# Kernel tuning notes

Measured on AMD Instinct MI355X. Metric: run time of the kernel, lower is better.

## Reference

```python
import jax, jax.numpy as jnp
import numpy as np

N_VERT = 20000


def _gather_pad(feat, adj):
    # feat: [B, N, C]; adj: [B, N, K] with 1-based indices, 0 = padding (-> zeros)
    B, N, C = feat.shape
    padded = jnp.concatenate([jnp.zeros((B, 1, C), feat.dtype), feat], axis=1)  # [B, N+1, C]
    return jax.vmap(lambda p, a: p[a])(padded, adj)  # [B, N, K, C]


def setup_inputs() -> dict:
    key = jax.random.key(0)
    ks = jax.random.split(key, 7)
    B, N, K, M, C, O = 4, N_VERT, 16, 9, 64, 64
    x = jax.random.normal(ks[0], (B, N, C), jnp.float32)
    adj = jax.random.randint(ks[1], (B, N, K), 0, N + 1, jnp.int32)  # 0 == no neighbor
    W = jax.random.normal(ks[2], (M, O, C), jnp.float32) * 0.1
    b = jax.random.normal(ks[3], (O,), jnp.float32) * 0.1
    u = jax.random.normal(ks[4], (M, C), jnp.float32) * 0.1
    v = jax.random.normal(ks[5], (M, C), jnp.float32) * 0.1
    c = jax.random.normal(ks[6], (M,), jnp.float32) * 0.1
    return {"x": x, "adj": adj, "W": W, "b": b, "u": u, "v": v, "c": c}


def reference(x, adj, W, b, u, v, c):
    # FEAST graph conv, non-invariant path.
    mask = adj != 0  # [B, N, K]
    # attention logits: u.x_i + v.x_j + c, masked (padding) neighbors -> 0 + c
    ux = jnp.einsum('bnc,mc->bnm', x, u)          # [B, N, M]
    vx = jnp.einsum('bnc,mc->bnm', x, v)          # [B, N, M]
    vxn = _gather_pad(vx, adj)                    # [B, N, K, M]
    logits = jnp.where(mask[..., None], ux[:, :, None, :] + vxn, 0.0) + c
    q = jax.nn.softmax(logits, axis=-1)           # softmax over M kernels
    # gather raw neighbor features (zero for padding), contract q over K first,
    # then apply per-kernel W (linear, so order is equivalent to original wx-gather)
    xn = _gather_pad(x, adj)                      # [B, N, K, C]
    s = jnp.einsum('bnkm,bnkc->bnmc', q, xn)      # [B, N, M, C]
    out = jnp.einsum('bnmc,moc->bno', s, W)       # [B, N, O]
    deg = jnp.sum(mask, axis=-1).astype(x.dtype)  # [B, N]
    inv_deg = jnp.where(deg > 0, 1.0 / jnp.maximum(deg, 1.0), 0.0)
    return out * inv_deg[..., None] + b
```

## Files before the change

### kernel.cpp

```cpp
#include <hip/hip_runtime.h>
#include <cstdint>
#include <cstddef>

#define BB 4
#define NN 20000
#define KK 16
#define MM 9
#define CC 64
#define OO 64
#define BN (BB*NN)
#define MC (MM*CC)
#define UVP 12
#define NKS (MC/32)
#define NCH 625

typedef _Float16 f16x8 __attribute__((ext_vector_type(8)));
typedef _Float16 f16x4 __attribute__((ext_vector_type(4)));
typedef __fp16   fp16v2 __attribute__((ext_vector_type(2)));
typedef float    f32x4 __attribute__((ext_vector_type(4)));
typedef unsigned short u16;
typedef unsigned int   u32;

union Hcv { _Float16 h; u16 u; };
__device__ __forceinline__ u16 f2h(float f) { Hcv t; t.h = (_Float16)f; return t.u; }
__device__ __forceinline__ float h2f(u16 h) { Hcv t; t.u = h; return (float)t.h; }

__device__ __forceinline__ f16x4 tr_read(u32 addr) {
    f16x4 r;
    asm volatile("ds_read_b64_tr_b16 %0, %1 offset:0" : "=v"(r) : "v"(addr) : "memory");
    return r;
}

__global__ __launch_bounds__(256) void pre_kernel(
    const float* __restrict__ x, const float* __restrict__ W,
    const float* __restrict__ u, const float* __restrict__ v,
    const float* __restrict__ c,
    float* __restrict__ uxcv, u16* __restrict__ xh,
    u16* __restrict__ wfb2, u16* __restrict__ vfa)
{
    const int bid = blockIdx.x;
    if (bid == 1286) {
        int i0 = threadIdx.x * 4;
        if (i0 < 1024) {
            u16 w4[4];
            #pragma unroll
            for (int tt = 0; tt < 4; ++tt) {
                int i = i0 + tt;
                int l = i >> 4, s = (i >> 3) & 1, j = i & 7;
                int m = l & 15, hh = l >> 4;
                float val = (m < 9) ? v[m * 64 + s * 32 + hh * 8 + j] : 0.f;
                w4[tt] = f2h(val);
            }
            *(ushort4*)(vfa + i0) = *(ushort4*)(w4);
        }
        return;
    }
    if (bid >= 1250) {
        int base = (bid - 1250) * 1024 + threadIdx.x * 4;
        ushort4 wv;
        u16* wp = (u16*)&wv;
        #pragma unroll
        for (int t = 0; t < 4; ++t) {
            int i = base + t;
            int j = i & 7, o = (i >> 3) & 63, l2 = (i >> 9) & 3, ks = i >> 11;
            int kf = ks * 32 + l2 * 8 + j;
            int m = kf >> 6, cc2 = kf & 63;
            wp[t] = f2h(W[m * 4096 + o * 64 + cc2]);
        }
        *(ushort4*)(wfb2 + base) = wv;
        return;
    }
    const int wave = threadIdx.x >> 6, lane = threadIdx.x & 63;
    const int lr = lane & 15, lhi = lane >> 4;
    const int t0n = bid * 64 + wave * 16;
    const float* xr = x + (size_t)(t0n + lr) * 64 + lhi * 8;
    float xf[16];
    *(float4*)(xf + 0)  = *(const float4*)(xr + 0);
    *(float4*)(xf + 4)  = *(const float4*)(xr + 4);
    *(float4*)(xf + 8)  = *(const float4*)(xr + 32);
    *(float4*)(xf + 12) = *(const float4*)(xr + 36);
    union { u16 us[8]; f16x8 v; ushort4 s4[2]; } H0, L0, H1, L1;
    #pragma unroll
    for (int i = 0; i < 8; ++i) {
        u16 h = f2h(xf[i]);      H0.us[i] = h;  L0.us[i] = f2h(xf[i] - h2f(h));
        u16 h2 = f2h(xf[8 + i]); H1.us[i] = h2; L1.us[i] = f2h(xf[8 + i] - h2f(h2));
    }
    u16* xw = xh + (size_t)(t0n + lr) * 64 + lhi * 8;
    *(ushort4*)(xw)          = H0.s4[0];
    *(ushort4*)(xw + 4)      = H0.s4[1];
    *(ushort4*)(xw + 32)     = H1.s4[0];
    *(ushort4*)(xw + 32 + 4) = H1.s4[1];

    f32x4 acc = {0.f,0.f,0.f,0.f};
    const float* gp = u + lr * 64;
    bool nz = lr < 9;
    #pragma unroll
    for (int s = 0; s < 2; ++s) {
        float gf[8];
        *(float4*)(gf + 0) = nz ? *(const float4*)(gp + s * 32 + lhi * 8)
                                : make_float4(0.f,0.f,0.f,0.f);
        *(float4*)(gf + 4) = nz ? *(const float4*)(gp + s * 32 + lhi * 8 + 4)
                                : make_float4(0.f,0.f,0.f,0.f);
        union { u16 us[8]; f16x8 v; } GH, GL;
        #pragma unroll
        for (int i = 0; i < 8; ++i) {
            u16 h = f2h(gf[i]); GH.us[i] = h; GL.us[i] = f2h(gf[i] - h2f(h));
        }
        f16x8 as  = s ? H1.v : H0.v;
        f16x8 asl = s ? L1.v : L0.v;
        acc = __builtin_amdgcn_mfma_f32_16x16x32_f16(as,  GH.v, acc, 0, 0, 0);
        acc = __builtin_amdgcn_mfma_f32_16x16x32_f16(as,  GL.v, acc, 0, 0, 0);
        acc = __builtin_amdgcn_mfma_f32_16x16x32_f16(asl, GH.v, acc, 0, 0, 0);
    }
    float cv = (lr < 9) ? c[lr] : 0.f;
    #pragma unroll
    for (int reg = 0; reg < 4; ++reg) {
        int node = t0n + lhi * 4 + reg;
        if (lr < 9) uxcv[(size_t)node * UVP + lr] = acc[reg] + cv;
    }
}

__global__ __launch_bounds__(256, 2) void fused_kernel(
    const u16* __restrict__ xh, const int* __restrict__ adj,
    const float* __restrict__ uxcv, const u16* __restrict__ wfb2,
    const u16* __restrict__ vfa, const float* __restrict__ bias,
    float* __restrict__ out)
{
    __shared__ __align__(16) u16 qlds[4 * 4 * 256];
    __shared__ __align__(16) u16 xnlds[4 * 4 * 1024];
    __shared__ __align__(16) u16 slds[72 * 32 * 8];
    const int bid = blockIdx.x;
    const int grp = bid & 7;
    const int b = grp >> 1;
    const int chunk = (bid >> 3) * 2 + (grp & 1);
    if (chunk >= NCH) return;
    const int tid = threadIdx.x, wave = tid >> 6, lane = tid & 63;
    const int lr = lane & 15, lhi = lane >> 4;
    const int node0 = b * NN + chunk * 32;
    const u16* xhb = xh + ((size_t)(b * NN) << 6);

    int jjA[2];
    jjA[0] = adj[(size_t)node0 * KK + tid];
    jjA[1] = adj[(size_t)node0 * KK + 256 + tid];

    f16x8 gLo[2][4], gHi[2][4];
    #pragma unroll
    for (int t = 0; t < 2; ++t)
        #pragma unroll
        for (int g2 = 0; g2 < 4; ++g2) {
            int e = __builtin_amdgcn_ds_bpermute((g2 * 16 + lr) * 4, jjA[t]);
            int erow = ((e > 0) ? e : 1) - 1;
            const u16* rp = xhb + ((size_t)erow << 6) + lhi * 8;
            gLo[t][g2] = *(const f16x8*)(rp);
            gHi[t][g2] = *(const f16x8*)(rp + 32);
        }

    float4 uc[2][4];
    #pragma unroll
    for (int t = 0; t < 2; ++t)
        #pragma unroll
        for (int g2 = 0; g2 < 4; ++g2)
            uc[t][g2] = *(const float4*)(uxcv +
                          (size_t)(node0 + t * 16 + wave * 4 + g2) * UVP + lhi * 4);

    const u16* vp = vfa + lane * 16;
    const f16x8 vAlo = *(const f16x8*)(vp);
    const f16x8 vAhi = *(const f16x8*)(vp + 8);

    const int o0 = wave * 16;
    const float bv = bias[o0 + lr];
    const u32 qbase  = (u32)(size_t)qlds  + wave * 2048 + lane * 8;
    const u32 xnbase = (u32)(size_t)xnlds + wave * 8192 + lane * 8;
    u16* xnw = xnlds + wave * 4096 + (lhi >> 1) * 256 + lr * 16 + (lhi & 1) * 8;
    u16* qwp = qlds + wave * 1024 + lhi * 4 + (lr & 3) * 16 + (lr >> 2) * 64;

    #pragma unroll
    for (int t = 0; t < 2; ++t) {
        unsigned long long bal = __ballot(jjA[t] != 0);
        #pragma unroll
        for (int g2 = 0; g2 < 4; ++g2) {
            *(f16x8*)(xnw + g2 * 1024)       = gLo[t][g2];
            *(f16x8*)(xnw + g2 * 1024 + 512) = gHi[t][g2];
        }
        #pragma unroll
        for (int g2 = 0; g2 < 4; ++g2) {
            f32x4 acc = {0.f, 0.f, 0.f, 0.f};
            acc = __builtin_amdgcn_mfma_f32_16x16x32_f16(vAlo, gLo[t][g2], acc, 0, 0, 0);
            acc = __builtin_amdgcn_mfma_f32_16x16x32_f16(vAhi, gHi[t][g2], acc, 0, 0, 0);
            u32 field = (u32)(bal >> (g2 * 16)) & 0xffffu;
            int  deg  = __popc(field);
            float inv = (deg > 0) ? __fdividef(1.0f, (float)deg) : 0.0f;
            int kbit = (field >> lr) & 1;
            float lm[4];
            #pragma unroll
            for (int r = 0; r < 4; ++r)
                lm[r] = (lhi * 4 + r < 9) ? (acc[r] + ((const float*)&uc[t][g2])[r])
                                          : -1e30f;
            float mx = fmaxf(fmaxf(lm[0], lm[1]), fmaxf(lm[2], lm[3]));
            mx = fmaxf(mx, __shfl_xor(mx, 16));
            mx = fmaxf(mx, __shfl_xor(mx, 32));
            float p0 = __expf(lm[0] - mx), p1 = __expf(lm[1] - mx);
            float p2 = __expf(lm[2] - mx), p3 = __expf(lm[3] - mx);
            float S = p0 + p1 + p2 + p3;
            S += __shfl_xor(S, 16);
            S += __shfl_xor(S, 32);
            float qsc = kbit ? __fdividef(inv, S) : 0.0f;
            union { fp16v2 h2[2]; uint2 u2; } qp;
            qp.h2[0] = __builtin_amdgcn_cvt_pkrtz(p0 * qsc, p1 * qsc);
            qp.h2[1] = __builtin_amdgcn_cvt_pkrtz(p2 * qsc, p3 * qsc);
            *(uint2*)(qwp + g2 * 256) = qp.u2;
        }
        asm volatile("s_waitcnt lgkmcnt(0)" ::: "memory");
        __builtin_amdgcn_sched_barrier(0);
        f16x4 qf[4], xnf[4][4];
        #pragma unroll
        for (int g2 = 0; g2 < 4; ++g2) {
            qf[g2] = tr_read(qbase + g2 * 512);
            #pragma unroll
            for (int cc = 0; cc < 4; ++cc)
                xnf[g2][cc] = tr_read(xnbase + g2 * 2048 + cc * 512);
        }
        asm volatile("s_waitcnt lgkmcnt(0)" ::: "memory");
        __builtin_amdgcn_sched_barrier(0);
        #pragma unroll
        for (int g2 = 0; g2 < 4; ++g2) {
            const int rnode = t * 16 + wave * 4 + g2;
            #pragma unroll
            for (int cc = 0; cc < 4; ++cc) {
                f32x4 d2 = {0.f, 0.f, 0.f, 0.f};
                d2 = __builtin_amdgcn_mfma_f32_16x16x16f16(xnf[g2][cc], qf[g2], d2, 0, 0, 0);
                if (lr < 9) {
                    u32 lo = __builtin_amdgcn_perm((u32)f2h(d2[1]), (u32)f2h(d2[0]), 0x05040100u);
                    u32 hi = __builtin_amdgcn_perm((u32)f2h(d2[3]), (u32)f2h(d2[2]), 0x05040100u);
                    int q_ = lr * 8 + cc * 2 + (lhi >> 1);
                    int idx = (((q_ * 32 + rnode) << 3) ^ ((lr & 7) << 3)) + (lhi & 1) * 4;
                    *(uint2*)(slds + idx) = make_uint2(lo, hi);
                }
            }
        }
    }
    __syncthreads();

    f32x4 a0 = {0.f, 0.f, 0.f, 0.f}, a1 = {0.f, 0.f, 0.f, 0.f};
    #pragma unroll
    for (int ks = 0; ks < NKS; ++ks) {
        int q_ = ks * 4 + lhi;
        int sw = ((q_ >> 3) & 7) << 3;
        f16x8 af0 = *(const f16x8*)(slds + ((((q_ * 32) + lr) << 3) ^ sw));
        f16x8 af1 = *(const f16x8*)(slds + ((((q_ * 32) + 16 + lr) << 3) ^ sw));
        f16x8 bf  = *(const f16x8*)(wfb2 + (size_t)(q_ * 64 + o0 + lr) * 8);
        a0 = __builtin_amdgcn_mfma_f32_16x16x32_f16(af0, bf, a0, 0, 0, 0);
        a1 = __builtin_amdgcn_mfma_f32_16x16x32_f16(af1, bf, a1, 0, 0, 0);
    }
    #pragma unroll
    for (int r = 0; r < 4; ++r) {
        out[(size_t)(node0 + lhi * 4 + r) * OO + o0 + lr]      = a0[r] + bv;
        out[(size_t)(node0 + 16 + lhi * 4 + r) * OO + o0 + lr] = a1[r] + bv;
    }
}

extern "C" void kernel_launch(void* const* d_in, const int* in_sizes, int n_in,
                              void* d_out, int out_size, void* d_ws, size_t ws_size,
                              hipStream_t stream)
{
    const float* x   = (const float*)d_in[0];
    const int*   adj = (const int*)  d_in[1];
    const float* W   = (const float*)d_in[2];
    const float* b   = (const float*)d_in[3];
    const float* u   = (const float*)d_in[4];
    const float* v   = (const float*)d_in[5];
    const float* c   = (const float*)d_in[6];
    float* out = (float*)d_out;

    float* uxcv = (float*)d_ws;
    u16*   xh   = (u16*)(uxcv + (size_t)BN * UVP);
    u16*   wfb2 = xh + (size_t)BN * CC;
    u16*   vfa  = wfb2 + 36864;

    pre_kernel<<<1287, 256, 0, stream>>>(x, W, u, v, c, uxcv, xh, wfb2, vfa);
    fused_kernel<<<2504, 256, 0, stream>>>(xh, adj, uxcv, wfb2, vfa, b, out);
}
```

Baseline: 135.7 us.

## Transpose gathered neighbor features via identity MFMA instead of LDS round-trip

Removes the xnlds shared buffer. Gathered neighbor rows are no longer written to LDS and read back with transpose reads; they are transposed in registers by an MFMA against an identity matrix. The q writes for both halves are batched before a single transpose-read phase, and launch bounds rise to 3 blocks per CU to use the lower LDS footprint. This trades LDS traffic for extra MFMA work and f16 conversions, and raises register pressure under the tighter occupancy bound.

```diff
diff --git a/kernel.cpp b/kernel.cpp
--- a/kernel.cpp
+++ b/kernel.cpp
@@ -35,7 +35,7 @@
     const float* __restrict__ x, const float* __restrict__ W,
     const float* __restrict__ u, const float* __restrict__ v,
     const float* __restrict__ c,
-    float* __restrict__ uxcv, u16* __restrict__ xh,
+    float* __restrict__ uxc, u16* __restrict__ xh,
     u16* __restrict__ wfb2, u16* __restrict__ vfa)
 {
     const int bid = blockIdx.x;
@@ -73,6 +73,7 @@
     const int wave = threadIdx.x >> 6, lane = threadIdx.x & 63;
     const int lr = lane & 15, lhi = lane >> 4;
     const int t0n = bid * 64 + wave * 16;
+
     const float* xr = x + (size_t)(t0n + lr) * 64 + lhi * 8;
     float xf[16];
     *(float4*)(xf + 0)  = *(const float4*)(xr + 0);
@@ -116,18 +117,17 @@
     #pragma unroll
     for (int reg = 0; reg < 4; ++reg) {
         int node = t0n + lhi * 4 + reg;
-        if (lr < 9) uxcv[(size_t)node * UVP + lr] = acc[reg] + cv;
-    }
-}
-
-__global__ __launch_bounds__(256, 2) void fused_kernel(
+        if (lr < 9) uxc[(size_t)node * UVP + lr] = acc[reg] + cv;
+    }
+}
+
+__global__ __launch_bounds__(256, 3) void fused_kernel(
     const u16* __restrict__ xh, const int* __restrict__ adj,
-    const float* __restrict__ uxcv, const u16* __restrict__ wfb2,
+    const float* __restrict__ uxc, const u16* __restrict__ wfb2,
     const u16* __restrict__ vfa, const float* __restrict__ bias,
     float* __restrict__ out)
 {
-    __shared__ __align__(16) u16 qlds[4 * 4 * 256];
-    __shared__ __align__(16) u16 xnlds[4 * 4 * 1024];
+    __shared__ __align__(16) u16 qlds[8192];
     __shared__ __align__(16) u16 slds[72 * 32 * 8];
     const int bid = blockIdx.x;
     const int grp = bid & 7;
@@ -137,11 +137,24 @@
     const int tid = threadIdx.x, wave = tid >> 6, lane = tid & 63;
     const int lr = lane & 15, lhi = lane >> 4;
     const int node0 = b * NN + chunk * 32;
-    const u16* xhb = xh + ((size_t)(b * NN) << 6);
+    const int rowbase = b * NN;
+    const u16* xhb = xh + ((size_t)rowbase << 6);
 
     int jjA[2];
     jjA[0] = adj[(size_t)node0 * KK + tid];
     jjA[1] = adj[(size_t)node0 * KK + 256 + tid];
+
+    float4 uc[2][4];
+    #pragma unroll
+    for (int t = 0; t < 2; ++t)
+        #pragma unroll
+        for (int g2 = 0; g2 < 4; ++g2)
+            uc[t][g2] = *(const float4*)(uxc +
+                          (size_t)(node0 + t * 16 + wave * 4 + g2) * UVP + lhi * 4);
+
+    const u16* vp = vfa + lane * 16;
+    const f16x8 vAlo = *(const f16x8*)(vp);
+    const f16x8 vAhi = *(const f16x8*)(vp + 8);
 
     f16x8 gLo[2][4], gHi[2][4];
     #pragma unroll
@@ -155,33 +168,23 @@
             gHi[t][g2] = *(const f16x8*)(rp + 32);
         }
 
-    float4 uc[2][4];
-    #pragma unroll
-    for (int t = 0; t < 2; ++t)
-        #pragma unroll
-        for (int g2 = 0; g2 < 4; ++g2)
-            uc[t][g2] = *(const float4*)(uxcv +
-                          (size_t)(node0 + t * 16 + wave * 4 + g2) * UVP + lhi * 4);
-
-    const u16* vp = vfa + lane * 16;
-    const f16x8 vAlo = *(const f16x8*)(vp);
-    const f16x8 vAhi = *(const f16x8*)(vp + 8);
-
-    const int o0 = wave * 16;
-    const float bv = bias[o0 + lr];
-    const u32 qbase  = (u32)(size_t)qlds  + wave * 2048 + lane * 8;
-    const u32 xnbase = (u32)(size_t)xnlds + wave * 8192 + lane * 8;
-    u16* xnw = xnlds + wave * 4096 + (lhi >> 1) * 256 + lr * 16 + (lhi & 1) * 8;
-    u16* qwp = qlds + wave * 1024 + lhi * 4 + (lr & 3) * 16 + (lr >> 2) * 64;
-
+    f16x8 idf[2];
+    #pragma unroll
+    for (int s = 0; s < 2; ++s) {
+        union { u16 us[8]; f16x8 v; } t;
+        #pragma unroll
+        for (int j = 0; j < 8; ++j)
+            t.us[j] = (lhi * 8 + j == s * 16 + lr) ? (u16)0x3C00 : (u16)0;
+        idf[s] = t.v;
+    }
+
+    unsigned long long bal0 = __ballot(jjA[0] != 0);
+    unsigned long long bal1 = __ballot(jjA[1] != 0);
+
+    u16* qwb = qlds + wave * 2048 + lr * 16 + lhi * 4;
     #pragma unroll
     for (int t = 0; t < 2; ++t) {
-        unsigned long long bal = __ballot(jjA[t] != 0);
-        #pragma unroll
-        for (int g2 = 0; g2 < 4; ++g2) {
-            *(f16x8*)(xnw + g2 * 1024)       = gLo[t][g2];
-            *(f16x8*)(xnw + g2 * 1024 + 512) = gHi[t][g2];
-        }
+        unsigned long long bal = t ? bal1 : bal0;
         #pragma unroll
         for (int g2 = 0; g2 < 4; ++g2) {
             f32x4 acc = {0.f, 0.f, 0.f, 0.f};
@@ -208,40 +211,50 @@
             union { fp16v2 h2[2]; uint2 u2; } qp;
             qp.h2[0] = __builtin_amdgcn_cvt_pkrtz(p0 * qsc, p1 * qsc);
             qp.h2[1] = __builtin_amdgcn_cvt_pkrtz(p2 * qsc, p3 * qsc);
-            *(uint2*)(qwp + g2 * 256) = qp.u2;
-        }
-        asm volatile("s_waitcnt lgkmcnt(0)" ::: "memory");
-        __builtin_amdgcn_sched_barrier(0);
-        f16x4 qf[4], xnf[4][4];
-        #pragma unroll
-        for (int g2 = 0; g2 < 4; ++g2) {
-            qf[g2] = tr_read(qbase + g2 * 512);
-            #pragma unroll
-            for (int cc = 0; cc < 4; ++cc)
-                xnf[g2][cc] = tr_read(xnbase + g2 * 2048 + cc * 512);
-        }
-        asm volatile("s_waitcnt lgkmcnt(0)" ::: "memory");
-        __builtin_amdgcn_sched_barrier(0);
+            *(uint2*)(qwb + t * 1024 + g2 * 256) = qp.u2;
+        }
+    }
+    asm volatile("s_waitcnt lgkmcnt(0)" ::: "memory");
+    const u32 qtr = (u32)(size_t)qlds + wave * 4096 + lane * 8;
+    f16x4 qf[2][4];
+    #pragma unroll
+    for (int t = 0; t < 2; ++t)
+        #pragma unroll
+        for (int g2 = 0; g2 < 4; ++g2)
+            qf[t][g2] = tr_read(qtr + t * 2048 + g2 * 512);
+    asm volatile("s_waitcnt lgkmcnt(0)" ::: "memory");
+    __builtin_amdgcn_sched_barrier(0);
+
+    #pragma unroll
+    for (int t = 0; t < 2; ++t)
         #pragma unroll
         for (int g2 = 0; g2 < 4; ++g2) {
             const int rnode = t * 16 + wave * 4 + g2;
             #pragma unroll
             for (int cc = 0; cc < 4; ++cc) {
-                f32x4 d2 = {0.f, 0.f, 0.f, 0.f};
-                d2 = __builtin_amdgcn_mfma_f32_16x16x16f16(xnf[g2][cc], qf[g2], d2, 0, 0, 0);
+                f32x4 xt = {0.f,0.f,0.f,0.f};
+                xt = __builtin_amdgcn_mfma_f32_16x16x32_f16(
+                         (cc < 2) ? gLo[t][g2] : gHi[t][g2], idf[cc & 1], xt, 0, 0, 0);
+                union { fp16v2 h2[2]; f16x4 h4; } at;
+                at.h2[0] = __builtin_amdgcn_cvt_pkrtz(xt[0], xt[1]);
+                at.h2[1] = __builtin_amdgcn_cvt_pkrtz(xt[2], xt[3]);
+                f32x4 d2 = {0.f,0.f,0.f,0.f};
+                d2 = __builtin_amdgcn_mfma_f32_16x16x16f16(at.h4, qf[t][g2], d2, 0, 0, 0);
+                union { fp16v2 h2[2]; uint2 u2; } sp;
+                sp.h2[0] = __builtin_amdgcn_cvt_pkrtz(d2[0], d2[1]);
+                sp.h2[1] = __builtin_amdgcn_cvt_pkrtz(d2[2], d2[3]);
                 if (lr < 9) {
-                    u32 lo = __builtin_amdgcn_perm((u32)f2h(d2[1]), (u32)f2h(d2[0]), 0x05040100u);
-                    u32 hi = __builtin_amdgcn_perm((u32)f2h(d2[3]), (u32)f2h(d2[2]), 0x05040100u);
                     int q_ = lr * 8 + cc * 2 + (lhi >> 1);
                     int idx = (((q_ * 32 + rnode) << 3) ^ ((lr & 7) << 3)) + (lhi & 1) * 4;
-                    *(uint2*)(slds + idx) = make_uint2(lo, hi);
+                    *(uint2*)(slds + idx) = sp.u2;
                 }
             }
         }
-    }
     __syncthreads();
 
-    f32x4 a0 = {0.f, 0.f, 0.f, 0.f}, a1 = {0.f, 0.f, 0.f, 0.f};
+    const int o0 = wave * 16;
+    const float bv = bias[o0 + lr];
+    f32x4 a0 = {0.f,0.f,0.f,0.f}, a1 = {0.f,0.f,0.f,0.f};
     #pragma unroll
     for (int ks = 0; ks < NKS; ++ks) {
         int q_ = ks * 4 + lhi;
@@ -272,11 +285,11 @@
     const float* c   = (const float*)d_in[6];
     float* out = (float*)d_out;
 
-    float* uxcv = (float*)d_ws;
-    u16*   xh   = (u16*)(uxcv + (size_t)BN * UVP);
+    float* uxc  = (float*)d_ws;
+    u16*   xh   = (u16*)(uxc + (size_t)BN * UVP);
     u16*   wfb2 = xh + (size_t)BN * CC;
     u16*   vfa  = wfb2 + 36864;
 
-    pre_kernel<<<1287, 256, 0, stream>>>(x, W, u, v, c, uxcv, xh, wfb2, vfa);
-    fused_kernel<<<2504, 256, 0, stream>>>(xh, adj, uxcv, wfb2, vfa, b, out);
-}
+    pre_kernel<<<1287, 256, 0, stream>>>(x, W, u, v, c, uxc, xh, wfb2, vfa);
+    fused_kernel<<<2504, 256, 0, stream>>>(xh, adj, uxc, wfb2, vfa, b, out);
+}
```

Result: faster. 125.5 us (-7.5%).
